# Performance work log

Measured on AMD Instinct MI355X. Metric: run time of the kernel, lower is better.

The kernel has to match this reference:

```python
import jax, jax.numpy as jnp
import numpy as np

B, D, N = 2, 256, 8192   # batch, in_channels, sequence length
CI = 128                 # inter_channels
BN_EPS = 1e-5


def conv1x1(w, b, x):
    # w: (Cout, Cin), b: (Cout,), x: (B, Cin, N) -> (B, Cout, N)
    return jnp.einsum('oc,bcn->bon', w, x) + b[None, :, None]


def maxpool2(x):
    # MaxPool1d(kernel_size=2): (B, C, N) -> (B, C, N//2)
    b, c, n = x.shape
    return x.reshape(b, c, n // 2, 2).max(axis=-1)


def setup_inputs() -> dict:
    key = jax.random.key(0)
    ks = jax.random.split(key, 11)
    s_in = 1.0 / np.sqrt(D)
    s_ci = 1.0 / np.sqrt(CI)
    return {
        'f': jax.random.normal(ks[0], (B, D, N), dtype=jnp.float32),
        'g_w': jax.random.uniform(ks[1], (CI, D), jnp.float32, -s_in, s_in),
        'g_b': jax.random.uniform(ks[2], (CI,), jnp.float32, -s_in, s_in),
        'theta_w': jax.random.uniform(ks[3], (CI, D), jnp.float32, -s_in, s_in),
        'theta_b': jax.random.uniform(ks[4], (CI,), jnp.float32, -s_in, s_in),
        'phi_w': jax.random.uniform(ks[5], (CI, D), jnp.float32, -s_in, s_in),
        'phi_b': jax.random.uniform(ks[6], (CI,), jnp.float32, -s_in, s_in),
        'W_w': jax.random.uniform(ks[7], (D, CI), jnp.float32, -s_ci, s_ci),
        'W_b': jax.random.uniform(ks[8], (D,), jnp.float32, -s_ci, s_ci),
        'bn_gamma': jax.random.normal(ks[9], (D,), dtype=jnp.float32) * 0.1,
        'bn_beta': jax.random.normal(ks[10], (D,), dtype=jnp.float32) * 0.1,
    }


def reference(f, g_w, g_b, theta_w, theta_b, phi_w, phi_b, W_w, W_b, bn_gamma, bn_beta):
    # projections (1x1 convs); g and phi are sub-sampled by maxpool(2)
    g_f = maxpool2(conv1x1(g_w, g_b, f))          # (B, CI, N/2)
    theta_f = conv1x1(theta_w, theta_b, f)        # (B, CI, N)
    phi_f = maxpool2(conv1x1(phi_w, phi_b, f))    # (B, CI, N/2)

    # affinity: theta^T @ phi, softmax over keys (no scale, as in source)
    A = jnp.einsum('bcn,bcm->bnm', theta_f, phi_f)     # (B, N, N/2)
    A = jax.nn.softmax(A, axis=-1)
    y = jnp.einsum('bnm,bcm->bcn', A, g_f)             # (B, CI, N)

    # W: 1x1 conv + BatchNorm1d (training-mode batch stats), residual
    Wy = conv1x1(W_w, W_b, y)                          # (B, D, N)
    mean = Wy.mean(axis=(0, 2), keepdims=True)
    var = Wy.var(axis=(0, 2), keepdims=True)           # biased, like torch BN
    Wy = (Wy - mean) * jax.lax.rsqrt(var + BN_EPS)
    Wy = Wy * bn_gamma[None, :, None] + bn_beta[None, :, None]
    return Wy + f
```

## Files before the change

kernel.cpp:

```cpp
#include <hip/hip_runtime.h>
#include <hip/hip_bf16.h>
#include <math.h>

#define B_ 2
#define D_ 256
#define N_ 8192
#define CI_ 128
#define M_ 4096
#define BN_EPS_ 1e-5f

#define OFF_WALL 0
#define OFF_THT  65536
#define OFF_PHT  (OFF_THT + 1048576)
#define OFF_GT   (OFF_PHT + 524288)
#define OFF_YP   (OFF_GT  + 524288)
#define OFF_ML   (OFF_YP  + 4194304)
#define OFF_MEAN (OFF_ML + 131072)
#define OFF_RSTD (OFF_MEAN + 256)

typedef __attribute__((ext_vector_type(8))) short bfrag;
typedef __attribute__((ext_vector_type(4))) float f4v;
typedef __attribute__((ext_vector_type(16))) float f16v;
typedef __attribute__((ext_vector_type(4))) short s4v;

__device__ inline unsigned short bf16rne(float x) {
    unsigned u = __float_as_uint(x);
    u += 0x7fff + ((u >> 16) & 1);
    return (unsigned short)(u >> 16);
}

__global__ __launch_bounds__(256) void wconv_kernel(
    const float* __restrict__ gw, const float* __restrict__ tw, const float* __restrict__ pw,
    const float* __restrict__ Ww, short* __restrict__ wall)
{
    int idx = blockIdx.x * 256 + threadIdx.x;
    int which = idx >> 15;
    int rem = idx & 32767;
    const float* src = (which == 0) ? gw : (which == 1) ? tw : (which == 2) ? pw : Ww;
    wall[idx] = (short)bf16rne(src[rem]);
}

__global__ __launch_bounds__(256, 2) void proj_kernel(
    const float* __restrict__ f, const short* __restrict__ wall,
    const float* __restrict__ tb, const float* __restrict__ gb, const float* __restrict__ pb,
    short* __restrict__ th_t, short* __restrict__ g_t, short* __restrict__ ph_t)
{
    __shared__ short sF[32 * 72];

    const int tid = threadIdx.x;
    const int wave = tid >> 6, lane = tid & 63;
    const int lq = lane & 15, quad = lane >> 4;
    const int b = blockIdx.y;
    const int n0 = blockIdx.x * 32;

    const float* fb = f + (size_t)b * D_ * N_;

    f4v acc[6][2];
#pragma unroll
    for (int ct = 0; ct < 6; ct++)
#pragma unroll
        for (int nf = 0; nf < 2; nf++) acc[ct][nf] = (f4v){0.f, 0.f, 0.f, 0.f};

    const int sn = tid & 31;
    const int sgrp = tid >> 5;

    for (int kc = 0; kc < D_; kc += 64) {
        __syncthreads();
#pragma unroll
        for (int jj = 0; jj < 4; jj++) {
            int dd = kc + sgrp * 8 + 2 * jj;
            float v0 = fb[(size_t)dd * N_ + n0 + sn];
            float v1 = fb[(size_t)(dd + 1) * N_ + n0 + sn];
            unsigned pk = (unsigned)bf16rne(v0) | ((unsigned)bf16rne(v1) << 16);
            *(unsigned*)&sF[sn * 72 + sgrp * 8 + 2 * jj] = pk;
        }
        __syncthreads();

        bfrag afr[6][2], bfr[2][2];
#pragma unroll
        for (int ks = 0; ks < 2; ks++) {
#pragma unroll
            for (int nf = 0; nf < 2; nf++)
                bfr[nf][ks] = *(const bfrag*)&sF[(nf * 16 + lq) * 72 + ks * 32 + quad * 8];
#pragma unroll
            for (int ct = 0; ct < 6; ct++)
                afr[ct][ks] = *(const bfrag*)&wall[(wave * 96 + ct * 16 + lq) * 256 + kc + ks * 32 + quad * 8];
        }
#pragma unroll
        for (int ks = 0; ks < 2; ks++)
#pragma unroll
            for (int ct = 0; ct < 6; ct++) {
                acc[ct][0] = __builtin_amdgcn_mfma_f32_16x16x32_bf16(afr[ct][ks], bfr[0][ks], acc[ct][0], 0, 0, 0);
                acc[ct][1] = __builtin_amdgcn_mfma_f32_16x16x32_bf16(afr[ct][ks], bfr[1][ks], acc[ct][1], 0, 0, 0);
            }
    }

#pragma unroll
    for (int ct = 0; ct < 6; ct++) {
        const int cf = wave * 6 + ct;
#pragma unroll
        for (int nf = 0; nf < 2; nf++) {
            f4v v = acc[ct][nf];
            const int n = n0 + nf * 16 + lq;
            if (cf < 8) {
                const int cb = cf * 16 + quad * 4;
                float pl[4];
#pragma unroll
                for (int r = 0; r < 4; r++) {
                    float o = __shfl_xor(v[r], 1);
                    pl[r] = fmaxf(v[r], o) + gb[cb + r];
                }
                if (!(lq & 1)) {
                    const int m = n >> 1;
#pragma unroll
                    for (int r = 0; r < 4; r++)
                        g_t[((size_t)b * CI_ + cb + r) * M_ + m] = (short)bf16rne(pl[r]);
                }
            } else if (cf < 16) {
                const int cb = (cf - 8) * 16 + quad * 4;
                s4v o;
#pragma unroll
                for (int r = 0; r < 4; r++) o[r] = (short)bf16rne(v[r] + tb[cb + r]);
                *(s4v*)&th_t[((size_t)b * N_ + n) * CI_ + cb] = o;
            } else {
                const int cb = (cf - 16) * 16 + quad * 4;
                float pl[4];
#pragma unroll
                for (int r = 0; r < 4; r++) {
                    float o = __shfl_xor(v[r], 1);
                    pl[r] = fmaxf(v[r], o) + pb[cb + r];
                }
                if (!(lq & 1)) {
                    const int m = n >> 1;
                    s4v o;
#pragma unroll
                    for (int r = 0; r < 4; r++) o[r] = (short)bf16rne(pl[r]);
                    *(s4v*)&ph_t[((size_t)b * M_ + m) * CI_ + cb] = o;
                }
            }
        }
    }
}

__global__ __launch_bounds__(256, 3) void attn_kernel(
    const short* __restrict__ th_p, const short* __restrict__ ph_p,
    const short* __restrict__ g_p, short* __restrict__ yp, float* __restrict__ ml)
{
    __shared__ short sPh[64 * 136];
    __shared__ short sG [128 * 72];

    const int tid = threadIdx.x;
    const int wave = tid >> 6, lane = tid & 63;
    const int l = lane & 31, h = lane >> 5;
    const int b = blockIdx.y, split = blockIdx.z;
    const int q0 = blockIdx.x * 128;
    const int qg = q0 + wave * 32 + l;

    const short* thr = th_p + ((size_t)b * N_ + qg) * CI_;
    bfrag tf[8];
#pragma unroll
    for (int s = 0; s < 8; s++)
        tf[s] = *(const bfrag*)&thr[s * 16 + h * 8];

    f16v yacc[4];
#pragma unroll
    for (int ct = 0; ct < 4; ct++)
#pragma unroll
        for (int r = 0; r < 16; r++) yacc[ct][r] = 0.f;
    float mI = -INFINITY, lI = 0.f;

    const short* phg = ph_p + (size_t)b * M_ * CI_;
    const short* gg  = g_p + (size_t)b * CI_ * M_;

    const int k0 = split * 1024;
    for (int kc = k0; kc < k0 + 1024; kc += 64) {
        __syncthreads();
#pragma unroll
        for (int p = 0; p < 4; p++) {
            int idx = p * 256 + tid;
            int r = idx >> 4, u = idx & 15;
            *(float4*)&sPh[r * 136 + u * 8] = *(const float4*)&phg[(size_t)(kc + r) * 128 + u * 8];
        }
#pragma unroll
        for (int p = 0; p < 4; p++) {
            int idx = p * 256 + tid;
            int r = idx >> 3, u = idx & 7;
            *(float4*)&sG[r * 72 + u * 8] = *(const float4*)&gg[(size_t)r * M_ + kc + u * 8];
        }
        __syncthreads();

        f16v sv[2];
#pragma unroll
        for (int kt = 0; kt < 2; kt++) {
            f16v a;
#pragma unroll
            for (int r = 0; r < 16; r++) a[r] = 0.f;
#pragma unroll
            for (int s = 0; s < 8; s++) {
                bfrag pa = *(const bfrag*)&sPh[(kt * 32 + l) * 136 + s * 16 + h * 8];
                a = __builtin_amdgcn_mfma_f32_32x32x16_bf16(pa, tf[s], a, 0, 0, 0);
            }
            sv[kt] = a;
        }

        float mx = sv[0][0];
#pragma unroll
        for (int kt = 0; kt < 2; kt++)
#pragma unroll
            for (int r = 0; r < 16; r++) mx = fmaxf(mx, sv[kt][r]);
        mx = fmaxf(mx, __shfl_xor(mx, 32));
        float mnew = fmaxf(mI, mx);
        float al = __expf(mI - mnew);
        float ps = 0.f;
        unsigned pu[16];
#pragma unroll
        for (int kt = 0; kt < 2; kt++)
#pragma unroll
            for (int i = 0; i < 8; i++) {
                int r = 2 * i;
                float p0 = __expf(sv[kt][r] - mnew);
                float p1 = __expf(sv[kt][r + 1] - mnew);
                ps += p0 + p1;
                pu[kt * 8 + (i >> 1) * 2 + (i & 1)] =
                    (unsigned)bf16rne(p0) | ((unsigned)bf16rne(p1) << 16);
            }
        ps += __shfl_xor(ps, 32);
        lI = lI * al + ps;
        mI = mnew;

        bfrag pf[4];
#pragma unroll
        for (int s = 0; s < 4; s++) {
            const int kt = s >> 1;
            const int iA = kt * 8 + ((2 * s) & 3) * 2;
            const int iB = kt * 8 + ((2 * s + 1) & 3) * 2;
            unsigned A0 = pu[iA], A1 = pu[iA + 1];
            unsigned B0 = pu[iB], B1 = pu[iB + 1];
            unsigned O0 = h ? B0 : A0;
            unsigned O1 = h ? B1 : A1;
            unsigned Xs0 = h ? A0 : B0;
            unsigned Xs1 = h ? A1 : B1;
            unsigned X0 = (unsigned)__shfl_xor((int)Xs0, 32);
            unsigned X1 = (unsigned)__shfl_xor((int)Xs1, 32);
            union { unsigned u[4]; bfrag v; } t;
            t.u[0] = h ? X0 : O0;
            t.u[1] = h ? X1 : O1;
            t.u[2] = h ? O0 : X0;
            t.u[3] = h ? O1 : X1;
            pf[s] = t.v;
        }

#pragma unroll
        for (int ct = 0; ct < 4; ct++)
#pragma unroll
            for (int r = 0; r < 16; r++) yacc[ct][r] *= al;

#pragma unroll
        for (int ct = 0; ct < 4; ct++)
#pragma unroll
            for (int s = 0; s < 4; s++) {
                bfrag ga = *(const bfrag*)&sG[(ct * 32 + l) * 72 + s * 16 + h * 8];
                yacc[ct] = __builtin_amdgcn_mfma_f32_32x32x16_bf16(ga, pf[s], yacc[ct], 0, 0, 0);
            }
    }

    short* yb = yp + (((size_t)split * B_ + b) * CI_) * N_;
#pragma unroll
    for (int ct = 0; ct < 4; ct++)
#pragma unroll
        for (int r = 0; r < 16; r++) {
            int c = ct * 32 + (r & 3) + 8 * (r >> 2) + 4 * h;
            yb[(size_t)c * N_ + qg] = (short)bf16rne(yacc[ct][r]);
        }
    if (h == 0) {
        float* mlb = ml + ((split * B_ + b) * 2) * N_;
        mlb[qg] = mI;
        mlb[N_ + qg] = lI;
    }
}

__global__ __launch_bounds__(256) void wy_merge_kernel(
    const short* __restrict__ yp, const float* __restrict__ ml,
    const short* __restrict__ wall2, const float* __restrict__ Wb,
    float* __restrict__ out)
{
    const int tid = threadIdx.x;
    const int wave = tid >> 6, lane = tid & 63;
    const int l = lane & 31, h = lane >> 5;
    const int b = blockIdx.y;
    const int n = blockIdx.x * 32 + l;

    float m[4], lv[4];
#pragma unroll
    for (int sp = 0; sp < 4; sp++) {
        const float* mlb = ml + ((sp * B_ + b) * 2) * N_;
        m[sp] = mlb[n];
        lv[sp] = mlb[N_ + n];
    }
    float mmax = fmaxf(fmaxf(m[0], m[1]), fmaxf(m[2], m[3]));
    float e[4], den = 0.f;
#pragma unroll
    for (int sp = 0; sp < 4; sp++) { e[sp] = __expf(m[sp] - mmax); den += lv[sp] * e[sp]; }
    float inv = 1.0f / den;
#pragma unroll
    for (int sp = 0; sp < 4; sp++) e[sp] *= inv;

    const unsigned short* ypu = (const unsigned short*)yp;
    bfrag by[8];
#pragma unroll
    for (int s = 0; s < 8; s++) {
#pragma unroll
        for (int j = 0; j < 8; j++) {
            const int c = s * 16 + h * 8 + j;
            float a = 0.f;
#pragma unroll
            for (int sp = 0; sp < 4; sp++) {
                unsigned short v = ypu[(((size_t)sp * B_ + b) * CI_ + c) * N_ + n];
                a = fmaf(e[sp], __uint_as_float((unsigned)v << 16), a);
            }
            by[s][j] = (short)bf16rne(a);
        }
    }

    f16v acc[2];
#pragma unroll
    for (int rt = 0; rt < 2; rt++)
#pragma unroll
        for (int r = 0; r < 16; r++) acc[rt][r] = 0.f;

#pragma unroll
    for (int s = 0; s < 8; s++)
#pragma unroll
        for (int rt = 0; rt < 2; rt++) {
            bfrag aw = *(const bfrag*)&wall2[((wave * 2 + rt) * 32 + l) * 128 + s * 16 + h * 8];
            acc[rt] = __builtin_amdgcn_mfma_f32_32x32x16_bf16(aw, by[s], acc[rt], 0, 0, 0);
        }

#pragma unroll
    for (int rt = 0; rt < 2; rt++)
#pragma unroll
        for (int r = 0; r < 16; r++) {
            const int d = (wave * 2 + rt) * 32 + (r & 3) + 8 * (r >> 2) + 4 * h;
            out[((size_t)b * D_ + d) * N_ + n] = acc[rt][r] + Wb[d];
        }
}

__global__ __launch_bounds__(256) void stats_kernel(
    const float* __restrict__ wy, float* __restrict__ mean, float* __restrict__ rstd)
{
    __shared__ float ssum[256], ssq[256];
    int d = blockIdx.x;
    int tid = threadIdx.x;
    float s = 0.f, sq = 0.f;
    for (int b = 0; b < B_; b++) {
        const float* p = wy + (size_t)b * D_ * N_ + (size_t)d * N_;
        for (int i = tid; i < N_; i += 256) {
            float v = p[i];
            s += v;
            sq = fmaf(v, v, sq);
        }
    }
    ssum[tid] = s; ssq[tid] = sq;
    __syncthreads();
    for (int st = 128; st > 0; st >>= 1) {
        if (tid < st) { ssum[tid] += ssum[tid + st]; ssq[tid] += ssq[tid + st]; }
        __syncthreads();
    }
    if (tid == 0) {
        float inv = 1.0f / (float)(B_ * N_);
        float mn = ssum[0] * inv;
        float var = ssq[0] * inv - mn * mn;
        mean[d] = mn;
        rstd[d] = rsqrtf(var + BN_EPS_);
    }
}

__global__ __launch_bounds__(256) void bn_res_kernel(
    float* __restrict__ out, const float* __restrict__ f,
    const float* __restrict__ mean, const float* __restrict__ rstd,
    const float* __restrict__ gamma, const float* __restrict__ beta)
{
    int i = blockIdx.x * 256 + threadIdx.x;
    size_t e = (size_t)i * 4;
    int d = (int)((e >> 13) & 255);
    float4 wy = ((const float4*)out)[i];
    float4 ff = ((const float4*)f)[i];
    float sc = rstd[d] * gamma[d];
    float mn = mean[d];
    float bt = beta[d];
    float4 r;
    r.x = (wy.x - mn) * sc + bt + ff.x;
    r.y = (wy.y - mn) * sc + bt + ff.y;
    r.z = (wy.z - mn) * sc + bt + ff.z;
    r.w = (wy.w - mn) * sc + bt + ff.w;
    ((float4*)out)[i] = r;
}

extern "C" void kernel_launch(void* const* d_in, const int* in_sizes, int n_in,
                              void* d_out, int out_size, void* d_ws, size_t ws_size,
                              hipStream_t stream)
{
    const float* f   = (const float*)d_in[0];
    const float* g_w = (const float*)d_in[1];
    const float* g_b = (const float*)d_in[2];
    const float* t_w = (const float*)d_in[3];
    const float* t_b = (const float*)d_in[4];
    const float* p_w = (const float*)d_in[5];
    const float* p_b = (const float*)d_in[6];
    const float* W_w = (const float*)d_in[7];
    const float* W_b = (const float*)d_in[8];
    const float* gam = (const float*)d_in[9];
    const float* bet = (const float*)d_in[10];
    float* out = (float*)d_out;
    float* ws = (float*)d_ws;

    short* wall  = (short*)(ws + OFF_WALL);
    short* wall2 = wall + 3 * 32768;
    short* th_t = (short*)(ws + OFF_THT);
    short* ph_t = (short*)(ws + OFF_PHT);
    short* g_t  = (short*)(ws + OFF_GT);
    short* ypart = (short*)(ws + OFF_YP);
    float* mlp = ws + OFF_ML;
    float* mnp = ws + OFF_MEAN;
    float* rsp = ws + OFF_RSTD;

    wconv_kernel<<<512, 256, 0, stream>>>(g_w, t_w, p_w, W_w, wall);
    proj_kernel<<<dim3(N_ / 32, B_), 256, 0, stream>>>(f, wall, t_b, g_b, p_b,
                                                       th_t, g_t, ph_t);
    attn_kernel<<<dim3(N_ / 128, B_, 4), 256, 0, stream>>>(th_t, ph_t, g_t, ypart, mlp);
    wy_merge_kernel<<<dim3(N_ / 32, B_), 256, 0, stream>>>(ypart, mlp, wall2, W_b, out);
    stats_kernel<<<D_, 256, 0, stream>>>(out, mnp, rsp);
    bn_res_kernel<<<(B_ * D_ * N_ / 4) / 256, 256, 0, stream>>>(out, f, mnp, rsp, gam, bet);
}
```

Before: 213.4 us.

## Prefetch next K tile into registers and store partial y as row-major

The attention kernel now loads the next phi/g tile from global memory into registers while the current tile is computed, double-buffering through registers. To fit the extra registers, the occupancy hint drops from 3 to 2 blocks. The partial y buffer is switched from channel-major to query-major layout, so the attention kernel writes 4-wide vectors and the merge kernel reads 16-byte vectors instead of scattered 2-byte loads. The tradeoff is lower occupancy in exchange for more latency hiding and coalesced stores and loads.

Result: slower. 256.3 us (+20.1%).

```diff
diff --git a/kernel.cpp b/kernel.cpp
--- a/kernel.cpp
+++ b/kernel.cpp
@@ -142,7 +142,7 @@
     }
 }
 
-__global__ __launch_bounds__(256, 3) void attn_kernel(
+__global__ __launch_bounds__(256, 2) void attn_kernel(
     const short* __restrict__ th_p, const short* __restrict__ ph_p,
     const short* __restrict__ g_p, short* __restrict__ yp, float* __restrict__ ml)
 {
@@ -156,6 +156,9 @@
     const int q0 = blockIdx.x * 128;
     const int qg = q0 + wave * 32 + l;
 
+    const int rp = tid >> 4, up = tid & 15;
+    const int rg = tid >> 3, ug = tid & 7;
+
     const short* thr = th_p + ((size_t)b * N_ + qg) * CI_;
     bfrag tf[8];
 #pragma unroll
@@ -173,19 +176,26 @@
     const short* gg  = g_p + (size_t)b * CI_ * M_;
 
     const int k0 = split * 1024;
+
+    float4 pfA[4], gfA[4];
+#pragma unroll
+    for (int p = 0; p < 4; p++) {
+        pfA[p] = *(const float4*)&phg[(size_t)(k0 + p * 16 + rp) * 128 + up * 8];
+        gfA[p] = *(const float4*)&gg[(size_t)(p * 32 + rg) * M_ + k0 + ug * 8];
+    }
+
     for (int kc = k0; kc < k0 + 1024; kc += 64) {
         __syncthreads();
 #pragma unroll
         for (int p = 0; p < 4; p++) {
-            int idx = p * 256 + tid;
-            int r = idx >> 4, u = idx & 15;
-            *(float4*)&sPh[r * 136 + u * 8] = *(const float4*)&phg[(size_t)(kc + r) * 128 + u * 8];
-        }
+            *(float4*)&sPh[(p * 16 + rp) * 136 + up * 8] = pfA[p];
+            *(float4*)&sG[(p * 32 + rg) * 72 + ug * 8] = gfA[p];
+        }
+        const int kn = (kc + 64 < k0 + 1024) ? kc + 64 : k0;
 #pragma unroll
         for (int p = 0; p < 4; p++) {
-            int idx = p * 256 + tid;
-            int r = idx >> 3, u = idx & 7;
-            *(float4*)&sG[r * 72 + u * 8] = *(const float4*)&gg[(size_t)r * M_ + kc + u * 8];
+            pfA[p] = *(const float4*)&phg[(size_t)(kn + p * 16 + rp) * 128 + up * 8];
+            gfA[p] = *(const float4*)&gg[(size_t)(p * 32 + rg) * M_ + kn + ug * 8];
         }
         __syncthreads();
 
@@ -264,13 +274,15 @@
             }
     }
 
-    short* yb = yp + (((size_t)split * B_ + b) * CI_) * N_;
+    short* yb = yp + (((size_t)split * B_ + b) * N_ + qg) * CI_;
 #pragma unroll
     for (int ct = 0; ct < 4; ct++)
 #pragma unroll
-        for (int r = 0; r < 16; r++) {
-            int c = ct * 32 + (r & 3) + 8 * (r >> 2) + 4 * h;
-            yb[(size_t)c * N_ + qg] = (short)bf16rne(yacc[ct][r]);
+        for (int a = 0; a < 4; a++) {
+            s4v o;
+#pragma unroll
+            for (int rr = 0; rr < 4; rr++) o[rr] = (short)bf16rne(yacc[ct][4 * a + rr]);
+            *(s4v*)&yb[ct * 32 + 8 * a + 4 * h] = o;
         }
     if (h == 0) {
         float* mlb = ml + ((split * B_ + b) * 2) * N_;
@@ -305,21 +317,23 @@
 #pragma unroll
     for (int sp = 0; sp < 4; sp++) e[sp] *= inv;
 
-    const unsigned short* ypu = (const unsigned short*)yp;
     bfrag by[8];
 #pragma unroll
     for (int s = 0; s < 8; s++) {
-#pragma unroll
-        for (int j = 0; j < 8; j++) {
-            const int c = s * 16 + h * 8 + j;
-            float a = 0.f;
-#pragma unroll
-            for (int sp = 0; sp < 4; sp++) {
-                unsigned short v = ypu[(((size_t)sp * B_ + b) * CI_ + c) * N_ + n];
-                a = fmaf(e[sp], __uint_as_float((unsigned)v << 16), a);
-            }
-            by[s][j] = (short)bf16rne(a);
-        }
+        float a8[8];
+#pragma unroll
+        for (int j = 0; j < 8; j++) a8[j] = 0.f;
+#pragma unroll
+        for (int sp = 0; sp < 4; sp++) {
+            bfrag v = *(const bfrag*)&yp[(((size_t)sp * B_ + b) * N_ + n) * CI_ + s * 16 + h * 8];
+#pragma unroll
+            for (int j = 0; j < 8; j++) {
+                float yv = __uint_as_float((unsigned)(unsigned short)v[j] << 16);
+                a8[j] = fmaf(e[sp], yv, a8[j]);
+            }
+        }
+#pragma unroll
+        for (int j = 0; j < 8; j++) by[s][j] = (short)bf16rne(a8[j]);
     }
 
     f16v acc[2];
```
